# Performance work log

Measured on AMD Instinct MI355X. Metric: run time of the kernel, lower is better.

The kernel has to match this reference:

```python
import jax, jax.numpy as jnp
import numpy as np
import math

D_MODEL = 1024
NUM_HEADS = 16
D_K = D_MODEL // NUM_HEADS


def setup_inputs() -> dict:
    key = jax.random.key(0)
    ks = jax.random.split(key, 9)
    s = 1.0 / math.sqrt(D_MODEL)
    x = jax.random.normal(ks[0], (2, 2048, D_MODEL), dtype=jnp.float32)
    # torch Linear params: weight [out, in], bias [out]
    Wq = jax.random.uniform(ks[1], (D_MODEL, D_MODEL), jnp.float32, -s, s)
    bq = jax.random.uniform(ks[2], (D_MODEL,), jnp.float32, -s, s)
    Wk = jax.random.uniform(ks[3], (D_MODEL, D_MODEL), jnp.float32, -s, s)
    bk = jax.random.uniform(ks[4], (D_MODEL,), jnp.float32, -s, s)
    Wv = jax.random.uniform(ks[5], (D_MODEL, D_MODEL), jnp.float32, -s, s)
    bv = jax.random.uniform(ks[6], (D_MODEL,), jnp.float32, -s, s)
    Wo = jax.random.uniform(ks[7], (D_MODEL, D_MODEL), jnp.float32, -s, s)
    bo = jax.random.uniform(ks[8], (D_MODEL,), jnp.float32, -s, s)
    return {"x": x, "Wq": Wq, "bq": bq, "Wk": Wk, "bk": bk,
            "Wv": Wv, "bv": bv, "Wo": Wo, "bo": bo}


def reference(x, Wq, bq, Wk, bk, Wv, bv, Wo, bo):
    B, T, _ = x.shape
    scale = 1.0 / math.sqrt(D_MODEL)  # NOTE: module scales by sqrt(d_model), not sqrt(d_k)

    def proj(W, b):
        # torch Linear: x @ W^T + b, then split heads -> [B, H, T, d_k]
        y = jnp.einsum('btd,ed->bte', x, W) + b
        return y.reshape(B, T, NUM_HEADS, D_K).transpose(0, 2, 1, 3)

    Q = proj(Wq, bq)
    K = proj(Wk, bk)
    V = proj(Wv, bv)
    logits = jnp.einsum('bhtd,bhsd->bhts', Q, K) * scale  # [B,H,T,T]
    attn = jax.nn.softmax(logits, axis=-1)
    out = jnp.einsum('bhts,bhsd->bhtd', attn, V)  # [B,H,T,d_k]
    out = out.transpose(0, 2, 1, 3).reshape(B, T, D_MODEL)
    return jnp.einsum('btd,ed->bte', out, Wo) + bo
```

## Files before the change

kernel.cpp:

```cpp
#include <hip/hip_runtime.h>

#define T_SEQ 2048
#define NB 2
#define NH 16
#define DK 64
#define DMODEL 1024

typedef __bf16 bf16x8 __attribute__((ext_vector_type(8)));
typedef float f32x4 __attribute__((ext_vector_type(4)));
typedef unsigned short ushortx8 __attribute__((ext_vector_type(8)));
typedef unsigned short ushortx4 __attribute__((ext_vector_type(4)));

__device__ inline unsigned short f2b1(float f) {
  unsigned u = __float_as_uint(f);
  u += 0x7fffu + ((u >> 16) & 1u);
  return (unsigned short)(u >> 16);
}

__device__ inline void gload16(const void* g, void* l) {
  __builtin_amdgcn_global_load_lds((const __attribute__((address_space(1))) void*)g,
                                   (__attribute__((address_space(3))) void*)l, 16, 0, 0);
}

__device__ inline bf16x8 mk8(unsigned a, unsigned b, unsigned c, unsigned d) {
  uint4 t = {a, b, c, d};
  return *(bf16x8*)&t;
}

__device__ inline unsigned cvtpk(float lo, float hi) {
  unsigned r;
  asm("v_cvt_pk_bf16_f32 %0, %1, %2" : "=v"(r) : "v"(lo), "v"(hi));
  return r;
}

__global__ void prep(const float* __restrict__ x,
                     const float* __restrict__ w0, const float* __restrict__ w1,
                     const float* __restrict__ w2, const float* __restrict__ w3,
                     const float* __restrict__ bq, const float* __restrict__ bk,
                     const float* __restrict__ bv,
                     unsigned short* __restrict__ xb, unsigned short* __restrict__ Wqkv,
                     float* __restrict__ bqkv) {
  int bid = blockIdx.x, tid = threadIdx.x;
  if (bid < 4096) {
    int i = (bid * 256 + tid) * 4;
    float4 v = *(const float4*)(x + i);
    ushortx4 o;
    o.x = f2b1(v.x); o.y = f2b1(v.y); o.z = f2b1(v.z); o.w = f2b1(v.w);
    *(ushortx4*)(xb + i) = o;
  } else if (bid < 8192) {
    int which = (bid - 4096) >> 10;
    int i = (((bid - 4096) & 1023) * 256 + tid) * 4;
    const float* src = which == 0 ? w0 : which == 1 ? w1 : which == 2 ? w2 : w3;
    float4 v = *(const float4*)(src + i);
    ushortx4 o;
    o.x = f2b1(v.x); o.y = f2b1(v.y); o.z = f2b1(v.z); o.w = f2b1(v.w);
    *(ushortx4*)(Wqkv + (long)which * 1048576 + i) = o;
  } else {
    int i = (bid - 8192) * 256 + tid;
    if (i < 3072) {
      float v = (i < 1024) ? bq[i] : (i < 2048 ? bk[i - 1024] : bv[i - 2048]);
      bqkv[i] = v;
    }
  }
}

__global__ __launch_bounds__(256, 3)
void gemm_qkv(const unsigned short* __restrict__ A, const unsigned short* __restrict__ B,
              const float* __restrict__ bias, unsigned short* __restrict__ Cb,
              unsigned short* __restrict__ Vt, int M, int N, int K, float scl) {
  __shared__ unsigned short As[2][4096];
  __shared__ unsigned short Bs[2][4096];
  const int tid = threadIdx.x;
  const int w = tid >> 6, lane = tid & 63;
  const int quad = lane >> 4, l16 = lane & 15;
  const int bm = blockIdx.y, bn = blockIdx.x;
  const int wm = w >> 1, wn = w & 1;

  f32x4 acc[4][4] = {};

  const int srow = tid >> 2;
  const int c4 = tid & 3;
  const unsigned short* aG = A + (long)(bm * 128 + srow) * K + c4 * 8;
  const unsigned short* bG = B + (long)(bn * 128 + srow) * K + c4 * 8;
  const long rs64 = (long)64 * K;
  const int wo = w * 512;

  gload16(aG, As[0] + wo);
  gload16(aG + rs64, As[0] + 2048 + wo);
  gload16(bG, Bs[0] + wo);
  gload16(bG + rs64, Bs[0] + 2048 + wo);

  int buf = 0;
  for (int kt = 0; kt < K; kt += 32) {
    __syncthreads();
    {
      const int nb = buf ^ 1;
      gload16(aG + kt + 32, As[nb] + wo);
      gload16(aG + rs64 + kt + 32, As[nb] + 2048 + wo);
      gload16(bG + kt + 32, Bs[nb] + wo);
      gload16(bG + rs64 + kt + 32, Bs[nb] + 2048 + wo);
    }

    bf16x8 af[4], bfr[4];
#pragma unroll
    for (int mt = 0; mt < 4; mt++)
      af[mt] = *(const bf16x8*)(As[buf] + (wm * 64 + mt * 16 + l16) * 32 + quad * 8);
#pragma unroll
    for (int nt = 0; nt < 4; nt++)
      bfr[nt] = *(const bf16x8*)(Bs[buf] + (wn * 64 + nt * 16 + l16) * 32 + quad * 8);
#pragma unroll
    for (int mt = 0; mt < 4; mt++)
#pragma unroll
      for (int nt = 0; nt < 4; nt++)
        acc[mt][nt] = __builtin_amdgcn_mfma_f32_16x16x32_bf16(af[mt], bfr[nt], acc[mt][nt], 0, 0, 0);
    buf ^= 1;
  }

  const int col0 = bn * 128 + wn * 64 + l16;
  const bool isV = (bn * 128) >= 2048;
#pragma unroll
  for (int mt = 0; mt < 4; mt++) {
    int row0 = bm * 128 + wm * 64 + mt * 16 + quad * 4;
#pragma unroll
    for (int nt = 0; nt < 4; nt++) {
      int col = col0 + nt * 16;
      float bb = bias[col];
      float s = (col < 1024) ? scl : 1.0f;
      if (!isV) {
#pragma unroll
        for (int r = 0; r < 4; r++)
          Cb[(long)(row0 + r) * N + col] = f2b1((acc[mt][nt][r] + bb) * s);
      } else {
        int cv = col - 2048;
        int h = cv >> 6, d = cv & 63;
        int b = row0 >> 11, t0 = row0 & 2047;
        int a = (t0 & 31) >> 2;
        int t0p = (t0 & ~31) | ((a & 3) << 3) | ((a >> 2) << 2);
        ushortx4 o;
        o.x = f2b1(acc[mt][nt][0] + bb);
        o.y = f2b1(acc[mt][nt][1] + bb);
        o.z = f2b1(acc[mt][nt][2] + bb);
        o.w = f2b1(acc[mt][nt][3] + bb);
        *(ushortx4*)(Vt + ((long)((b * NH + h) * DK + d)) * T_SEQ + t0p) = o;
      }
    }
  }
}

__global__ __launch_bounds__(256, 2)
void gemm_out(const unsigned short* __restrict__ A, const unsigned short* __restrict__ B,
              const float* __restrict__ bias, float* __restrict__ Cf, int M, int N, int K) {
  __shared__ unsigned short As[2][2048];
  __shared__ unsigned short Bs[2][4096];
  const int tid = threadIdx.x;
  const int w = tid >> 6, lane = tid & 63;
  const int quad = lane >> 4, l16 = lane & 15;
  const int bm = blockIdx.y, bn = blockIdx.x;
  const int wm = w >> 1, wn = w & 1;

  f32x4 acc[2][4] = {};

  const int srow = tid >> 2;
  const int c4 = tid & 3;
  const unsigned short* aG = A + (long)(bm * 64 + srow) * K + c4 * 8;
  const unsigned short* bG = B + (long)(bn * 128 + srow) * K + c4 * 8;
  const long rs64 = (long)64 * K;
  const int wo = w * 512;

  gload16(aG, As[0] + wo);
  gload16(bG, Bs[0] + wo);
  gload16(bG + rs64, Bs[0] + 2048 + wo);

  int buf = 0;
  for (int kt = 0; kt < K; kt += 32) {
    __syncthreads();
    {
      const int nb = buf ^ 1;
      gload16(aG + kt + 32, As[nb] + wo);
      gload16(bG + kt + 32, Bs[nb] + wo);
      gload16(bG + rs64 + kt + 32, Bs[nb] + 2048 + wo);
    }

    bf16x8 af[2], bfr[4];
#pragma unroll
    for (int mt = 0; mt < 2; mt++)
      af[mt] = *(const bf16x8*)(As[buf] + (wm * 32 + mt * 16 + l16) * 32 + quad * 8);
#pragma unroll
    for (int nt = 0; nt < 4; nt++)
      bfr[nt] = *(const bf16x8*)(Bs[buf] + (wn * 64 + nt * 16 + l16) * 32 + quad * 8);
#pragma unroll
    for (int mt = 0; mt < 2; mt++)
#pragma unroll
      for (int nt = 0; nt < 4; nt++)
        acc[mt][nt] = __builtin_amdgcn_mfma_f32_16x16x32_bf16(af[mt], bfr[nt], acc[mt][nt], 0, 0, 0);
    buf ^= 1;
  }

  const int col0 = bn * 128 + wn * 64 + l16;
#pragma unroll
  for (int mt = 0; mt < 2; mt++) {
    int row0 = bm * 64 + wm * 32 + mt * 16 + quad * 4;
#pragma unroll
    for (int nt = 0; nt < 4; nt++) {
      int col = col0 + nt * 16;
      float bb = bias[col];
#pragma unroll
      for (int r = 0; r < 4; r++)
        Cf[(long)(row0 + r) * N + col] = acc[mt][nt][r] + bb;
    }
  }
}


#define ATTN_BODY(IT, STP, STC)                                               \
  {                                                                           \
    const int cur = (IT) & 1;                                                 \
    __syncthreads();                                                          \
    if ((IT) < 31) {                                                          \
      const int nb = cur ^ 1;                                                 \
      gload16(kG[0], Ks[nb] + wo2);                                           \
      gload16(kG[1], Ks[nb] + wo2 + 512);                                     \
      gload16(vG[0], Vs[nb] + wo2);                                           \
      gload16(vG[1], Vs[nb] + wo2 + 512);                                     \
      kG[0] += 64 * 3072; kG[1] += 64 * 3072;                                 \
      vG[0] += 64;        vG[1] += 64;                                        \
    }                                                                         \
    bf16x8 pa[2][2];                                                          \
    _Pragma("unroll")                                                         \
    for (int g = 0; g < 2; g++) {                                             \
      unsigned pk[4][2];                                                      \
      _Pragma("unroll")                                                       \
      for (int nt = 0; nt < 4; nt++) {                                        \
        float p0 = __builtin_amdgcn_exp2f(STP[g][nt][0]);                     \
        float p1 = __builtin_amdgcn_exp2f(STP[g][nt][1]);                     \
        float p2 = __builtin_amdgcn_exp2f(STP[g][nt][2]);                     \
        float p3 = __builtin_amdgcn_exp2f(STP[g][nt][3]);                     \
        pk[nt][0] = cvtpk(p0, p1);                                            \
        pk[nt][1] = cvtpk(p2, p3);                                            \
      }                                                                       \
      pa[g][0] = mk8(pk[0][0], pk[0][1], pk[1][0], pk[1][1]);                 \
      pa[g][1] = mk8(pk[2][0], pk[2][1], pk[3][0], pk[3][1]);                 \
    }                                                                         \
    __builtin_amdgcn_s_setprio(1);                                            \
    _Pragma("unroll")                                                         \
    for (int nt = 0; nt < 4; nt++) {                                          \
      const char* kr = (char*)(Ks[cur]) + (nt * 16 + l16) * 128;              \
      bf16x8 k0 = *(const bf16x8*)(kr + ((quad * 16) ^ e16));                 \
      bf16x8 k1 = *(const bf16x8*)(kr + (((quad + 4) * 16) ^ e16));           \
      _Pragma("unroll")                                                       \
      for (int g = 0; g < 2; g++) {                                           \
        f32x4 z = {};                                                         \
        z = __builtin_amdgcn_mfma_f32_16x16x32_bf16(k0, qf[g][0], z, 0, 0, 0);\
        z = __builtin_amdgcn_mfma_f32_16x16x32_bf16(k1, qf[g][1], z, 0, 0, 0);\
        STC[g][nt] = z;                                                       \
      }                                                                       \
    }                                                                         \
    _Pragma("unroll")                                                         \
    for (int g = 0; g < 2; g++) {                                             \
      accp[g] = __builtin_amdgcn_mfma_f32_16x16x32_bf16(pa[g][0], ones, accp[g], 0, 0, 0); \
      accp[g] = __builtin_amdgcn_mfma_f32_16x16x32_bf16(pa[g][1], ones, accp[g], 0, 0, 0); \
    }                                                                         \
    _Pragma("unroll")                                                         \
    for (int nt = 0; nt < 4; nt++)                                            \
      _Pragma("unroll")                                                       \
      for (int km = 0; km < 2; km++)                                          \
        _Pragma("unroll")                                                     \
        for (int g = 0; g < 2; g++)                                           \
          acco[g][nt] = __builtin_amdgcn_mfma_f32_16x16x32_bf16(pa[g][km], vreg[nt][km], acco[g][nt], 0, 0, 0); \
    __builtin_amdgcn_s_setprio(0);                                            \
    _Pragma("unroll")                                                         \
    for (int nt = 0; nt < 4; nt++) {                                          \
      const char* vr = (char*)(Vs[cur]) + (nt * 16 + l16) * 128;              \
      _Pragma("unroll")                                                       \
      for (int km = 0; km < 2; km++)                                          \
        vreg[nt][km] = *(const bf16x8*)(vr + (((km * 4 + quad) * 16) ^ e16)); \
    }                                                                         \
  }

__global__ __launch_bounds__(256, 2)
void attn3(const unsigned short* __restrict__ QKV, const unsigned short* __restrict__ Vt,
           unsigned short* __restrict__ Ob) {
  __shared__ unsigned short Ks[2][4096];
  __shared__ unsigned short Vs[2][4096];
  const int tid = threadIdx.x;
  const int w = tid >> 6, lane = tid & 63;
  const int quad = lane >> 4, l16 = lane & 15;

  const int id = blockIdx.x;
  const int bh = id & 31;
  const int qt = id >> 5;
  const int b = bh >> 4, h = bh & 15;
  const long qkvBase = (long)b * T_SEQ * 3072;

  bf16x8 qf[2][2];
#pragma unroll
  for (int g = 0; g < 2; g++) {
    const unsigned short* qp = QKV + qkvBase + (long)(qt * 128 + w * 32 + g * 16 + l16) * 3072 + h * 64 + quad * 8;
    qf[g][0] = *(const bf16x8*)qp;
    qf[g][1] = *(const bf16x8*)(qp + 32);
  }

  const unsigned short* kG[2];
  const unsigned short* vG[2];
#pragma unroll
  for (int i = 0; i < 2; i++) {
    int S = w * 128 + i * 64 + lane;
    int row = S >> 3;
    int c = (S & 7) ^ (row & 7);
    kG[i] = QKV + qkvBase + 1024 + h * 64 + (long)row * 3072 + c * 8;
    vG[i] = Vt + (long)bh * DK * T_SEQ + (long)row * T_SEQ + c * 8;
  }
  const int wo2 = w * 1024;

  const unsigned onesu = 0x3F803F80u;
  const bf16x8 ones = mk8(onesu, onesu, onesu, onesu);

  f32x4 acco[2][4] = {};
  f32x4 accp[2] = {};
  bf16x8 vreg[4][2];
  f32x4 stA[2][4], stB[2][4];
  const int e16 = (l16 & 7) * 16;

  gload16(kG[0], Ks[0] + wo2);
  gload16(kG[1], Ks[0] + wo2 + 512);
  gload16(vG[0], Vs[0] + wo2);
  gload16(vG[1], Vs[0] + wo2 + 512);
  kG[0] += 64 * 3072; kG[1] += 64 * 3072;
  vG[0] += 64;        vG[1] += 64;
  __syncthreads();
  gload16(kG[0], Ks[1] + wo2);
  gload16(kG[1], Ks[1] + wo2 + 512);
  gload16(vG[0], Vs[1] + wo2);
  gload16(vG[1], Vs[1] + wo2 + 512);
  kG[0] += 64 * 3072; kG[1] += 64 * 3072;
  vG[0] += 64;        vG[1] += 64;
#pragma unroll
  for (int nt = 0; nt < 4; nt++) {
    const char* kr = (char*)(Ks[0]) + (nt * 16 + l16) * 128;
    bf16x8 k0 = *(const bf16x8*)(kr + ((quad * 16) ^ e16));
    bf16x8 k1 = *(const bf16x8*)(kr + (((quad + 4) * 16) ^ e16));
#pragma unroll
    for (int g = 0; g < 2; g++) {
      f32x4 z = {};
      z = __builtin_amdgcn_mfma_f32_16x16x32_bf16(k0, qf[g][0], z, 0, 0, 0);
      z = __builtin_amdgcn_mfma_f32_16x16x32_bf16(k1, qf[g][1], z, 0, 0, 0);
      stA[g][nt] = z;
    }
  }
#pragma unroll
  for (int nt = 0; nt < 4; nt++) {
    const char* vr = (char*)(Vs[0]) + (nt * 16 + l16) * 128;
#pragma unroll
    for (int km = 0; km < 2; km++)
      vreg[nt][km] = *(const bf16x8*)(vr + (((km * 4 + quad) * 16) ^ e16));
  }

#pragma unroll 1
  for (int it = 1; it < 31; it += 2) {
    ATTN_BODY(it, stA, stB);
    ATTN_BODY(it + 1, stB, stA);
  }
  ATTN_BODY(31, stA, stB);

  {
    bf16x8 pa[2][2];
#pragma unroll
    for (int g = 0; g < 2; g++) {
      unsigned pk[4][2];
#pragma unroll
      for (int nt = 0; nt < 4; nt++) {
        float p0 = __builtin_amdgcn_exp2f(stB[g][nt][0]);
        float p1 = __builtin_amdgcn_exp2f(stB[g][nt][1]);
        float p2 = __builtin_amdgcn_exp2f(stB[g][nt][2]);
        float p3 = __builtin_amdgcn_exp2f(stB[g][nt][3]);
        pk[nt][0] = cvtpk(p0, p1);
        pk[nt][1] = cvtpk(p2, p3);
      }
      pa[g][0] = mk8(pk[0][0], pk[0][1], pk[1][0], pk[1][1]);
      pa[g][1] = mk8(pk[2][0], pk[2][1], pk[3][0], pk[3][1]);
      accp[g] = __builtin_amdgcn_mfma_f32_16x16x32_bf16(pa[g][0], ones, accp[g], 0, 0, 0);
      accp[g] = __builtin_amdgcn_mfma_f32_16x16x32_bf16(pa[g][1], ones, accp[g], 0, 0, 0);
    }
#pragma unroll
    for (int nt = 0; nt < 4; nt++)
#pragma unroll
      for (int km = 0; km < 2; km++)
#pragma unroll
        for (int g = 0; g < 2; g++)
          acco[g][nt] = __builtin_amdgcn_mfma_f32_16x16x32_bf16(pa[g][km], vreg[nt][km], acco[g][nt], 0, 0, 0);
  }

  const int t0 = qt * 128 + w * 32;
#pragma unroll
  for (int g = 0; g < 2; g++) {
    f32x4 rl;
#pragma unroll
    for (int r = 0; r < 4; r++) rl[r] = __builtin_amdgcn_rcpf(accp[g][r]);
#pragma unroll
    for (int nt = 0; nt < 4; nt++)
#pragma unroll
      for (int r = 0; r < 4; r++) {
        int t = t0 + g * 16 + quad * 4 + r;
        Ob[(long)(b * T_SEQ + t) * DMODEL + h * 64 + nt * 16 + l16] = f2b1(acco[g][nt][r] * rl[r]);
      }
  }
}

extern "C" void kernel_launch(void* const* d_in, const int* in_sizes, int n_in,
                              void* d_out, int out_size, void* d_ws, size_t ws_size,
                              hipStream_t stream) {
  const float* x  = (const float*)d_in[0];
  const float* Wq = (const float*)d_in[1];
  const float* bq = (const float*)d_in[2];
  const float* Wk = (const float*)d_in[3];
  const float* bk = (const float*)d_in[4];
  const float* Wv = (const float*)d_in[5];
  const float* bv = (const float*)d_in[6];
  const float* Wo = (const float*)d_in[7];
  const float* bo = (const float*)d_in[8];
  float* out = (float*)d_out;

  unsigned short* xb   = (unsigned short*)d_ws;
  unsigned short* Wqkv = xb + 4194304;
  unsigned short* Wob  = Wqkv + 3145728;
  float*          bqkv = (float*)(Wob + 1048576);
  unsigned short* QKV  = (unsigned short*)(bqkv + 3072);
  unsigned short* Vt   = QKV + 12582912;
  unsigned short* Ob   = Vt + 4194304;

  prep<<<8204, 256, 0, stream>>>(x, Wq, Wk, Wv, Wo, bq, bk, bv, xb, Wqkv, bqkv);

  gemm_qkv<<<dim3(24, 32), 256, 0, stream>>>(xb, Wqkv, bqkv, QKV, Vt,
                                             4096, 3072, 1024, 0.04508422037f);

  attn3<<<dim3(512), 256, 0, stream>>>(QKV, Vt, Ob);

  gemm_out<<<dim3(8, 64), 256, 0, stream>>>(Ob, Wob, bo, out, 4096, 1024, 1024);
}
```

Before: 178.0 us.

## Triple-buffer K/V tiles in attention with vmcnt-based waits

Switches the attention kernel's K/V shared-memory staging from double to triple buffering, so loads run two tiles ahead of compute. The full __syncthreads drain is replaced by an explicit s_waitcnt vmcnt(4) plus a raw barrier, which lets the newest tile's loads stay in flight across the barrier. This aims to hide more global-load latency behind the MFMA work. In exchange, LDS use per block rises from 32KB to 48KB, and the buffer index becomes a runtime modulo-3.

After: 182.6 us. +2.6%, slower.

```diff
diff --git a/kernel.cpp b/kernel.cpp
--- a/kernel.cpp
+++ b/kernel.cpp
@@ -212,12 +212,14 @@
 }
 
 
-#define ATTN_BODY(IT, STP, STC)                                               \
+#define ATTN_BODY(IT, STP, STC, WAITSTR)                                      \
   {                                                                           \
-    const int cur = (IT) & 1;                                                 \
-    __syncthreads();                                                          \
-    if ((IT) < 31) {                                                          \
-      const int nb = cur ^ 1;                                                 \
+    const int cur3 = (IT) % 3;                                                \
+    asm volatile(WAITSTR ::: "memory");                                       \
+    __builtin_amdgcn_s_barrier();                                             \
+    __builtin_amdgcn_sched_barrier(0);                                        \
+    if ((IT) < 30) {                                                          \
+      const int nb = ((IT) + 2) % 3;                                          \
       gload16(kG[0], Ks[nb] + wo2);                                           \
       gload16(kG[1], Ks[nb] + wo2 + 512);                                     \
       gload16(vG[0], Vs[nb] + wo2);                                           \
@@ -244,7 +246,7 @@
     __builtin_amdgcn_s_setprio(1);                                            \
     _Pragma("unroll")                                                         \
     for (int nt = 0; nt < 4; nt++) {                                          \
-      const char* kr = (char*)(Ks[cur]) + (nt * 16 + l16) * 128;              \
+      const char* kr = (char*)(Ks[cur3]) + (nt * 16 + l16) * 128;             \
       bf16x8 k0 = *(const bf16x8*)(kr + ((quad * 16) ^ e16));                 \
       bf16x8 k1 = *(const bf16x8*)(kr + (((quad + 4) * 16) ^ e16));           \
       _Pragma("unroll")                                                       \
@@ -270,7 +272,7 @@
     __builtin_amdgcn_s_setprio(0);                                            \
     _Pragma("unroll")                                                         \
     for (int nt = 0; nt < 4; nt++) {                                          \
-      const char* vr = (char*)(Vs[cur]) + (nt * 16 + l16) * 128;              \
+      const char* vr = (char*)(Vs[cur3]) + (nt * 16 + l16) * 128;             \
       _Pragma("unroll")                                                       \
       for (int km = 0; km < 2; km++)                                          \
         vreg[nt][km] = *(const bf16x8*)(vr + (((km * 4 + quad) * 16) ^ e16)); \
@@ -280,8 +282,8 @@
 __global__ __launch_bounds__(256, 2)
 void attn3(const unsigned short* __restrict__ QKV, const unsigned short* __restrict__ Vt,
            unsigned short* __restrict__ Ob) {
-  __shared__ unsigned short Ks[2][4096];
-  __shared__ unsigned short Vs[2][4096];
+  __shared__ unsigned short Ks[3][4096];
+  __shared__ unsigned short Vs[3][4096];
   const int tid = threadIdx.x;
   const int w = tid >> 6, lane = tid & 63;
   const int quad = lane >> 4, l16 = lane & 15;
@@ -327,13 +329,21 @@
   gload16(vG[1], Vs[0] + wo2 + 512);
   kG[0] += 64 * 3072; kG[1] += 64 * 3072;
   vG[0] += 64;        vG[1] += 64;
-  __syncthreads();
   gload16(kG[0], Ks[1] + wo2);
   gload16(kG[1], Ks[1] + wo2 + 512);
   gload16(vG[0], Vs[1] + wo2);
   gload16(vG[1], Vs[1] + wo2 + 512);
   kG[0] += 64 * 3072; kG[1] += 64 * 3072;
   vG[0] += 64;        vG[1] += 64;
+  asm volatile("s_waitcnt vmcnt(4)" ::: "memory");
+  __builtin_amdgcn_s_barrier();
+  __builtin_amdgcn_sched_barrier(0);
+  gload16(kG[0], Ks[2] + wo2);
+  gload16(kG[1], Ks[2] + wo2 + 512);
+  gload16(vG[0], Vs[2] + wo2);
+  gload16(vG[1], Vs[2] + wo2 + 512);
+  kG[0] += 64 * 3072; kG[1] += 64 * 3072;
+  vG[0] += 64;        vG[1] += 64;
 #pragma unroll
   for (int nt = 0; nt < 4; nt++) {
     const char* kr = (char*)(Ks[0]) + (nt * 16 + l16) * 128;
@@ -357,10 +367,10 @@
 
 #pragma unroll 1
   for (int it = 1; it < 31; it += 2) {
-    ATTN_BODY(it, stA, stB);
-    ATTN_BODY(it + 1, stB, stA);
-  }
-  ATTN_BODY(31, stA, stB);
+    ATTN_BODY(it, stA, stB, "s_waitcnt vmcnt(4) lgkmcnt(0)");
+    ATTN_BODY(it + 1, stB, stA, "s_waitcnt vmcnt(4) lgkmcnt(0)");
+  }
+  ATTN_BODY(31, stA, stB, "s_waitcnt vmcnt(0) lgkmcnt(0)");
 
   {
     bf16x8 pa[2][2];
```
